# Performance work log

Measured on AMD Instinct MI355X. Metric: run time of the kernel, lower is better.

The kernel has to match this reference:

```python
import jax, jax.numpy as jnp
import numpy as np


def setup_inputs() -> dict:
    key = jax.random.key(0)
    k1, k2, k3 = jax.random.split(key, 3)
    B, C_IN, C_OUT, R, K = 4, 64, 64, 64, 3
    x = jax.random.normal(k1, (B, C_IN, R, R, R), dtype=jnp.float32)
    # per-voxel nonzero test |x|.sum(channel) != 0 used by the module)
    keep = jax.random.uniform(k2, (B, 1, R, R, R)) < 0.3
    x = x * keep.astype(jnp.float32)
    weight = jax.random.normal(k3, (C_OUT, C_IN, K, K, K), dtype=jnp.float32)
    return {"x": x, "weight": weight}


def reference(x, weight):
    # The torch module gathers a k^3 neighborhood at every nonzero input voxel,
    # contracts with the (unflipped) weight, and scatters to the same voxel.
    # This is exactly cross-correlation (torch conv semantics) with SAME padding,
    # masked to voxels where the input is nonzero across channels.
    K = weight.shape[-1]
    pad_l = K // 2
    pad_r = K - 1 - pad_l
    out = jax.lax.conv_general_dilated(
        x, weight,
        window_strides=(1, 1, 1),
        padding=[(pad_l, pad_r)] * 3,
        dimension_numbers=("NCDHW", "OIDHW", "NCDHW"),
    )  # [B, C_out, D, H, W]
    mask = (jnp.abs(x).sum(axis=1, keepdims=True) != 0)  # [B,1,D,H,W]
    return out * mask.astype(out.dtype)
```

## Files before the change

kernel.cpp:

```cpp
#include <hip/hip_runtime.h>
#include <stdint.h>


#define R3 262144
#define NVOX (4 * R3)
#define P  66
#define PS (66 * 66)
#define PB (66 * 66 * 66)
#define WSW_ELEMS (27 * 2 * 4 * 64 * 8)
#define CAP (NVOX / 2)

typedef __attribute__((ext_vector_type(4))) float f32x4;
typedef __attribute__((ext_vector_type(8))) short short8;

static __device__ inline unsigned short f2bf(float f) {
    union { float f; unsigned u; } v; v.f = f;
    unsigned u = v.u;
    return (unsigned short)((u + 0x7fffu + ((u >> 16) & 1u)) >> 16);
}

static __device__ __forceinline__ void gload16(const void* g, void* l) {
    __builtin_amdgcn_global_load_lds(
        (const __attribute__((address_space(1))) unsigned int*)g,
        (__attribute__((address_space(3))) unsigned int*)l, 16, 0, 0);
}

__global__ void wprep(const float* __restrict__ w, unsigned short* __restrict__ wsw) {
    int e = blockIdx.x * 256 + threadIdx.x;
    if (e >= WSW_ELEMS) return;
    int j    = e & 7;
    int lane = (e >> 3) & 63;
    int nt   = (e >> 9) & 3;
    int kc   = (e >> 11) & 1;
    int tap  = e >> 12;
    int co = nt * 16 + (lane & 15);
    int ci = kc * 32 + ((lane >> 4) * 8) + j;
    wsw[e] = f2bf(w[(co * 64 + ci) * 27 + tap]);
}

__global__ void __launch_bounds__(256) halo_zero(uint4* __restrict__ xt4) {
    int p = blockIdx.x * 256 + threadIdx.x;
    if (p >= 4 * PB) return;
    int b = p / PB;
    int rp = p - b * PB;
    int z = rp / PS; rp -= z * PS;
    int y = rp / P;  int xx = rp - y * P;
    if (z == 0 || z == 65 || y == 0 || y == 65 || xx == 0 || xx == 65) {
        uint4 zz = {0, 0, 0, 0};
        uint4* d = xt4 + (size_t)p * 8;
#pragma unroll
        for (int k = 0; k < 8; ++k) d[k] = zz;
    }
}

__global__ void __launch_bounds__(256) xprep(const float* __restrict__ x,
                                             unsigned int* __restrict__ xt_u32,
                                             int* __restrict__ list,
                                             int* __restrict__ pos,
                                             int* __restrict__ count) {
    __shared__ unsigned int lds[256 * 36];
    __shared__ unsigned int wcnt[4], wbase[4], bbase;
    int t = threadIdx.x;
    int v = blockIdx.x * 256 + t;
    int b = v >> 18;
    int s = v & (R3 - 1);
    const float* xb = x + (size_t)b * (64 * R3) + s;
    bool active = false;
    unsigned int pk[32];
#pragma unroll
    for (int c2 = 0; c2 < 32; ++c2) {
        float f0 = xb[(size_t)(2 * c2) * R3];
        float f1 = xb[(size_t)(2 * c2 + 1) * R3];
        active |= (f0 != 0.f) | (f1 != 0.f);
        pk[c2] = (unsigned)f2bf(f0) | ((unsigned)f2bf(f1) << 16);
    }
#pragma unroll
    for (int k = 0; k < 8; ++k) {
        uint4 q = { pk[4 * k], pk[4 * k + 1], pk[4 * k + 2], pk[4 * k + 3] };
        *(uint4*)&lds[t * 36 + 4 * k] = q;
    }
    __syncthreads();
    int s0 = (blockIdx.x * 256) & (R3 - 1);
    int z0 = s0 >> 12;
    int y0 = (s0 >> 6) & 63;
    size_t rowbase = ((size_t)b * PB + (size_t)(z0 + 1) * PS + (size_t)(y0 + 1) * P + 1) * 32;
#pragma unroll
    for (int i = 0; i < 8; ++i) {
        int g4 = i * 256 + t;
        int vox = g4 >> 3;
        int col = (g4 & 7) * 4;
        uint4 val = *(const uint4*)&lds[vox * 36 + col];
        int r = vox >> 6;
        int xc = vox & 63;
        *(uint4*)&xt_u32[rowbase + (size_t)r * (P * 32) + (size_t)xc * 32 + col] = val;
    }
    int lane = t & 63, w = t >> 6;
    unsigned long long bal = __ballot(active);
    if (lane == 0) wcnt[w] = (unsigned)__popcll(bal);
    __syncthreads();
    if (t == 0) {
        unsigned tot = 0;
        for (int i = 0; i < 4; ++i) { wbase[i] = tot; tot += wcnt[i]; }
        bbase = (unsigned)atomicAdd(count, (int)tot);
    }
    __syncthreads();
    int p = -1;
    if (active) {
        unsigned pp = bbase + wbase[w] + (unsigned)__popcll(bal & ((1ULL << lane) - 1ULL));
        list[pp] = v;
        p = (int)pp;
    }
    pos[v] = p;
}

#define AST(tp, sl) do { if ((tp) < 27) {                                           \
    const int dz_ = (tp) / 9 - 1, dy_ = ((tp) / 3) % 3 - 1, dx_ = (tp) % 3 - 1;     \
    const ptrdiff_t dlt_ = (ptrdiff_t)(dz_ * PS + dy_ * P + dx_) * 128;             \
    _Pragma("unroll")                                                               \
    for (int i_ = 0; i_ < 4; ++i_)                                                  \
        gload16(asrc[i_] + dlt_, aw + (sl) * 4096 + i_ * 1024 + lane * 16);         \
    asm volatile("" ::: "memory");                                                  \
} } while (0)

#define BLD(tp, st) do { if ((tp) < 27) {                                           \
    _Pragma("unroll")                                                               \
    for (int j_ = 0; j_ < 8; ++j_)                                                  \
        breg[st][j_] = *(const short8*)(wswb + (size_t)(tp) * 8192 + j_ * 1024      \
                                        + lane * 16);                               \
    asm volatile("" ::: "memory");                                                  \
} } while (0)

__global__ void __launch_bounds__(256, 3) sconv_gemm(const unsigned char* __restrict__ xt,
                                                     const unsigned char* __restrict__ wswb,
                                                     const int* __restrict__ list,
                                                     const int* __restrict__ count_p,
                                                     float* __restrict__ out,
                                                     float* __restrict__ compact,
                                                     int use_compact) {
    __shared__ __align__(16) unsigned char Ab[4][3][4096];
    int count = *count_p;
    int nt_act = (count + 127) >> 7;
    int bid = blockIdx.x;
    if (bid >= nt_act) return;
    int qd = nt_act >> 3, rd = nt_act & 7;
    int xcd = bid & 7, ixx = bid >> 3;
    int tile = (xcd < rd ? xcd * (qd + 1) : rd * (qd + 1) + (xcd - rd) * qd) + ixx;
    int base = tile * 128;
    int t = threadIdx.x;
    int lane = t & 63, w = t >> 6;

    const unsigned char* asrc[4];
    {
        int seg = lane & 7;
        int rl0 = lane >> 3;
        int off = (seg * 16) ^ ((rl0 & 7) << 4);
#pragma unroll
        for (int i = 0; i < 4; ++i) {
            int gi = base + w * 32 + rl0 + 8 * i;
            int vid = (gi < count) ? list[gi] : 0;
            if (vid < 0) vid = 0;
            int bb = vid >> 18, sp = vid & (R3 - 1);
            int vz = sp >> 12, vy = (sp >> 6) & 63, vx = sp & 63;
            size_t pvox = (size_t)bb * PB + (size_t)(vz + 1) * PS + (size_t)(vy + 1) * P + (vx + 1);
            asrc[i] = xt + pvox * 128 + off;
        }
    }
    unsigned char* aw = &Ab[w][0][0];

    int cl = lane & 15;
    int hi16 = (lane >> 4) * 16;
    int aoff[2][2];
#pragma unroll
    for (int m = 0; m < 2; ++m)
#pragma unroll
        for (int kc = 0; kc < 2; ++kc)
            aoff[m][kc] = (m * 16 + cl) * 128 + ((kc * 64 + hi16) ^ ((cl & 7) << 4));

    f32x4 acc[2][4] = {};
    short8 breg[2][8];

    BLD(0, 0);
    AST(0, 0);
    AST(1, 1);
#pragma unroll
    for (int tp = 0; tp < 27; ++tp) {
        const int sl = tp % 3;
        const int st = tp & 1;
        if (tp == 0)       asm volatile("s_waitcnt vmcnt(4)"  ::: "memory");
        else if (tp < 26)  asm volatile("s_waitcnt vmcnt(12)" ::: "memory");
        else               asm volatile("s_waitcnt vmcnt(8)"  ::: "memory");
        short8 a0k0 = *(const short8*)(aw + sl * 4096 + aoff[0][0]);
        short8 a1k0 = *(const short8*)(aw + sl * 4096 + aoff[1][0]);
        short8 a0k1 = *(const short8*)(aw + sl * 4096 + aoff[0][1]);
        short8 a1k1 = *(const short8*)(aw + sl * 4096 + aoff[1][1]);
        BLD(tp + 1, st ^ 1);
        AST(tp + 2, (tp + 2) % 3);
#pragma unroll
        for (int n = 0; n < 4; ++n) {
            acc[0][n] = __builtin_amdgcn_mfma_f32_16x16x32_bf16(a0k0, breg[st][n], acc[0][n], 0, 0, 0);
            acc[1][n] = __builtin_amdgcn_mfma_f32_16x16x32_bf16(a1k0, breg[st][n], acc[1][n], 0, 0, 0);
        }
#pragma unroll
        for (int n = 0; n < 4; ++n) {
            acc[0][n] = __builtin_amdgcn_mfma_f32_16x16x32_bf16(a0k1, breg[st][4 + n], acc[0][n], 0, 0, 0);
            acc[1][n] = __builtin_amdgcn_mfma_f32_16x16x32_bf16(a1k1, breg[st][4 + n], acc[1][n], 0, 0, 0);
        }
        asm volatile("s_waitcnt lgkmcnt(0)" ::: "memory");
    }

    int q = lane >> 4;
    if (use_compact) {
#pragma unroll
        for (int m = 0; m < 2; ++m) {
#pragma unroll
            for (int rg = 0; rg < 4; ++rg) {
                int row = w * 32 + m * 16 + q * 4 + rg;
                int gi = base + row;
                if (gi < count && gi < CAP) {
#pragma unroll
                    for (int n = 0; n < 4; ++n)
                        compact[(size_t)gi * 64 + n * 16 + cl] = acc[m][n][rg];
                }
            }
        }
    } else {
#pragma unroll
        for (int m = 0; m < 2; ++m) {
#pragma unroll
            for (int rg = 0; rg < 4; ++rg) {
                int row = w * 32 + m * 16 + q * 4 + rg;
                int gi = base + row;
                if (gi < count) {
                    int vv = list[gi];
                    int bb2 = vv >> 18;
                    int sp = vv & (R3 - 1);
                    float* op = out + (size_t)(bb2 * 64 + cl) * R3 + sp;
#pragma unroll
                    for (int n = 0; n < 4; ++n)
                        op[(size_t)(n * 16) * R3] = acc[m][n][rg];
                }
            }
        }
    }
}

__global__ void __launch_bounds__(256) finalize(const uint4* __restrict__ compact4,
                                                const int* __restrict__ pos,
                                                float* __restrict__ out) {
    int t = threadIdx.x;
    int vb = blockIdx.x * 256;
    int b = vb >> 18;
    int sp0 = vb & (R3 - 1);
    int q = pos[vb + t];
    bool act = (unsigned)q < (unsigned)CAP;
    const uint4* src = compact4 + (size_t)(act ? q : 0) * 16;
    uint4 r[16];
#pragma unroll
    for (int s = 0; s < 16; ++s) {
        uint4 v = {0, 0, 0, 0};
        if (act) v = src[s];
        r[s] = v;
    }
    const float* rf = (const float*)r;
    float* ob = out + (size_t)b * 64 * R3 + sp0 + t;
#pragma unroll
    for (int co = 0; co < 64; ++co)
        ob[(size_t)co * R3] = rf[co];
}

__global__ void __launch_bounds__(64) fallback_conv(const float* __restrict__ x,
                                                    const float* __restrict__ wt,
                                                    float* __restrict__ out) {
    __shared__ float rowb[66];
    int bid = blockIdx.x;
    int y = bid & 63, z = (bid >> 6) & 63, co = (bid >> 12) & 63, b = bid >> 18;
    int t = threadIdx.x;
    float acc = 0.f;
    bool active = false;
    for (int ci = 0; ci < 64; ++ci) {
        const float* xp = x + ((size_t)(b * 64 + ci)) * R3;
        const float* wp = wt + ((size_t)(co * 64 + ci)) * 27;
        for (int dz = -1; dz <= 1; ++dz) {
            int nz = z + dz;
            bool okz = (unsigned)nz < 64u;
            for (int dy = -1; dy <= 1; ++dy) {
                int ny = y + dy;
                bool ok = okz && ((unsigned)ny < 64u);
                float v = ok ? xp[nz * 4096 + ny * 64 + t] : 0.f;
                rowb[t + 1] = v;
                if (t == 0) { rowb[0] = 0.f; rowb[65] = 0.f; }
                __syncthreads();
                if (dz == 0 && dy == 0) active |= (rowb[t + 1] != 0.f);
                const float* wq = wp + (dz + 1) * 9 + (dy + 1) * 3;
                acc += rowb[t] * wq[0] + rowb[t + 1] * wq[1] + rowb[t + 2] * wq[2];
                __syncthreads();
            }
        }
    }
    out[((size_t)(b * 64 + co)) * R3 + z * 4096 + y * 64 + t] = active ? acc : 0.f;
}

extern "C" void kernel_launch(void* const* d_in, const int* in_sizes, int n_in,
                              void* d_out, int out_size, void* d_ws, size_t ws_size,
                              hipStream_t stream) {
    const float* x = (const float*)d_in[0];
    const float* w = (const float*)d_in[1];
    float* out = (float*)d_out;

    const size_t XT_BYTES = (size_t)4 * PB * 128;
    const size_t LIST_OFF = XT_BYTES;
    const size_t POS_OFF  = LIST_OFF + (size_t)NVOX * 4;
    const size_t WSW_OFF  = POS_OFF + (size_t)NVOX * 4;
    const size_t CNT_OFF  = WSW_OFF + (size_t)WSW_ELEMS * 2;
    const size_t CMP_OFF  = (CNT_OFF + 256 + 255) & ~(size_t)255;
    const size_t NEED_S   = CMP_OFF;
    const size_t NEED_C   = CMP_OFF + (size_t)CAP * 64 * 4;

    if (ws_size < NEED_S) {
        fallback_conv<<<NVOX, 64, 0, stream>>>(x, w, out);
        return;
    }

    unsigned int*   xt   = (unsigned int*)d_ws;
    int*            list = (int*)((char*)d_ws + LIST_OFF);
    int*            pos  = (int*)((char*)d_ws + POS_OFF);
    unsigned short* wsw  = (unsigned short*)((char*)d_ws + WSW_OFF);
    int*            cnt  = (int*)((char*)d_ws + CNT_OFF);
    float*          cmp  = (float*)((char*)d_ws + CMP_OFF);
    int use_compact = (ws_size >= NEED_C) ? 1 : 0;

    hipMemsetAsync(cnt, 0, sizeof(int), stream);
    if (!use_compact)
        hipMemsetAsync(d_out, 0, (size_t)out_size * sizeof(float), stream);
    wprep<<<WSW_ELEMS / 256, 256, 0, stream>>>(w, wsw);
    halo_zero<<<(4 * PB + 255) / 256, 256, 0, stream>>>((uint4*)d_ws);
    xprep<<<NVOX / 256, 256, 0, stream>>>(x, xt, list, pos, cnt);
    sconv_gemm<<<NVOX / 128, 256, 0, stream>>>((const unsigned char*)xt,
                                               (const unsigned char*)wsw, list, cnt,
                                               out, cmp, use_compact);
    if (use_compact)
        finalize<<<NVOX / 256, 256, 0, stream>>>((const uint4*)cmp, pos, out);
}
```

Baseline: 683.0 us.

## Load A operands directly from global into registers, dropping LDS staging

The gathered activation rows are now loaded straight from global memory into MFMA operand registers with a three-slot register ring, in place of async global-to-LDS copies followed by LDS reads. Both A and B use a prefetch distance of two taps, and the manual vmcnt/lgkmcnt waits are removed, leaving scheduling to the compiler. This removes LDS traffic, the swizzle and the per-tap barriers-by-waitcnt, at the cost of more VGPRs: launch bounds drop from 3 to 2 blocks per SIMD, and the per-lane gather loads may be less coalesced.

Measured after the change: 730.1 us. +6.9%, slower.

```diff
diff --git a/kernel.cpp b/kernel.cpp
--- a/kernel.cpp
+++ b/kernel.cpp
@@ -17,12 +17,6 @@
     union { float f; unsigned u; } v; v.f = f;
     unsigned u = v.u;
     return (unsigned short)((u + 0x7fffu + ((u >> 16) & 1u)) >> 16);
-}
-
-static __device__ __forceinline__ void gload16(const void* g, void* l) {
-    __builtin_amdgcn_global_load_lds(
-        (const __attribute__((address_space(1))) unsigned int*)g,
-        (__attribute__((address_space(3))) unsigned int*)l, 16, 0, 0);
 }
 
 __global__ void wprep(const float* __restrict__ w, unsigned short* __restrict__ wsw) {
@@ -113,31 +107,31 @@
     pos[v] = p;
 }
 
-#define AST(tp, sl) do { if ((tp) < 27) {                                           \
+#define ALOAD(tp, sl) do { if ((tp) < 27) {                                         \
     const int dz_ = (tp) / 9 - 1, dy_ = ((tp) / 3) % 3 - 1, dx_ = (tp) % 3 - 1;     \
-    const ptrdiff_t dlt_ = (ptrdiff_t)(dz_ * PS + dy_ * P + dx_) * 128;             \
+    const int dlt_ = (dz_ * PS + dy_ * P + dx_) * 128;                              \
     _Pragma("unroll")                                                               \
-    for (int i_ = 0; i_ < 4; ++i_)                                                  \
-        gload16(asrc[i_] + dlt_, aw + (sl) * 4096 + i_ * 1024 + lane * 16);         \
-    asm volatile("" ::: "memory");                                                  \
+    for (int m_ = 0; m_ < 2; ++m_)                                                  \
+    _Pragma("unroll")                                                               \
+    for (int kc_ = 0; kc_ < 2; ++kc_)                                               \
+        a[sl][m_][kc_] = *(const short8*)(xt +                                      \
+            (size_t)(voffA[m_] + (unsigned)(dlt_ + kc_ * 64)));                     \
 } } while (0)
 
-#define BLD(tp, st) do { if ((tp) < 27) {                                           \
+#define BLOAD(tp, sl) do { if ((tp) < 27) {                                         \
     _Pragma("unroll")                                                               \
     for (int j_ = 0; j_ < 8; ++j_)                                                  \
-        breg[st][j_] = *(const short8*)(wswb + (size_t)(tp) * 8192 + j_ * 1024      \
-                                        + lane * 16);                               \
-    asm volatile("" ::: "memory");                                                  \
+        b[sl][j_] = *(const short8*)(wswb + (size_t)((tp) * 8192 + j_ * 1024)       \
+                                     + voffB);                                      \
 } } while (0)
 
-__global__ void __launch_bounds__(256, 3) sconv_gemm(const unsigned char* __restrict__ xt,
+__global__ void __launch_bounds__(256, 2) sconv_gemm(const unsigned char* __restrict__ xt,
                                                      const unsigned char* __restrict__ wswb,
                                                      const int* __restrict__ list,
                                                      const int* __restrict__ count_p,
                                                      float* __restrict__ out,
                                                      float* __restrict__ compact,
                                                      int use_compact) {
-    __shared__ __align__(16) unsigned char Ab[4][3][4096];
     int count = *count_p;
     int nt_act = (count + 127) >> 7;
     int bid = blockIdx.x;
@@ -145,67 +139,45 @@
     int qd = nt_act >> 3, rd = nt_act & 7;
     int xcd = bid & 7, ixx = bid >> 3;
     int tile = (xcd < rd ? xcd * (qd + 1) : rd * (qd + 1) + (xcd - rd) * qd) + ixx;
-    int base = tile * 128;
     int t = threadIdx.x;
     int lane = t & 63, w = t >> 6;
-
-    const unsigned char* asrc[4];
-    {
-        int seg = lane & 7;
-        int rl0 = lane >> 3;
-        int off = (seg * 16) ^ ((rl0 & 7) << 4);
-#pragma unroll
-        for (int i = 0; i < 4; ++i) {
-            int gi = base + w * 32 + rl0 + 8 * i;
-            int vid = (gi < count) ? list[gi] : 0;
-            if (vid < 0) vid = 0;
-            int bb = vid >> 18, sp = vid & (R3 - 1);
-            int vz = sp >> 12, vy = (sp >> 6) & 63, vx = sp & 63;
-            size_t pvox = (size_t)bb * PB + (size_t)(vz + 1) * PS + (size_t)(vy + 1) * P + (vx + 1);
-            asrc[i] = xt + pvox * 128 + off;
-        }
-    }
-    unsigned char* aw = &Ab[w][0][0];
-
+    int base = tile * 128 + w * 32;
     int cl = lane & 15;
     int hi16 = (lane >> 4) * 16;
-    int aoff[2][2];
-#pragma unroll
-    for (int m = 0; m < 2; ++m)
-#pragma unroll
-        for (int kc = 0; kc < 2; ++kc)
-            aoff[m][kc] = (m * 16 + cl) * 128 + ((kc * 64 + hi16) ^ ((cl & 7) << 4));
+
+    unsigned voffA[2];
+#pragma unroll
+    for (int m = 0; m < 2; ++m) {
+        int gi = base + m * 16 + cl;
+        int vid = (gi < count) ? list[gi] : 0;
+        int bb = vid >> 18, sp = vid & (R3 - 1);
+        int vz = sp >> 12, vy = (sp >> 6) & 63, vx = sp & 63;
+        voffA[m] = (unsigned)((bb * PB + (vz + 1) * PS + (vy + 1) * P + (vx + 1)) * 128)
+                   + (unsigned)hi16;
+    }
+    unsigned voffB = (unsigned)(lane * 16);
 
     f32x4 acc[2][4] = {};
-    short8 breg[2][8];
-
-    BLD(0, 0);
-    AST(0, 0);
-    AST(1, 1);
+    short8 a[3][2][2];
+    short8 b[3][8];
+
+    BLOAD(0, 0); ALOAD(0, 0);
+    BLOAD(1, 1); ALOAD(1, 1);
 #pragma unroll
     for (int tp = 0; tp < 27; ++tp) {
         const int sl = tp % 3;
-        const int st = tp & 1;
-        if (tp == 0)       asm volatile("s_waitcnt vmcnt(4)"  ::: "memory");
-        else if (tp < 26)  asm volatile("s_waitcnt vmcnt(12)" ::: "memory");
-        else               asm volatile("s_waitcnt vmcnt(8)"  ::: "memory");
-        short8 a0k0 = *(const short8*)(aw + sl * 4096 + aoff[0][0]);
-        short8 a1k0 = *(const short8*)(aw + sl * 4096 + aoff[1][0]);
-        short8 a0k1 = *(const short8*)(aw + sl * 4096 + aoff[0][1]);
-        short8 a1k1 = *(const short8*)(aw + sl * 4096 + aoff[1][1]);
-        BLD(tp + 1, st ^ 1);
-        AST(tp + 2, (tp + 2) % 3);
+        BLOAD(tp + 2, (tp + 2) % 3);
+        ALOAD(tp + 2, (tp + 2) % 3);
 #pragma unroll
         for (int n = 0; n < 4; ++n) {
-            acc[0][n] = __builtin_amdgcn_mfma_f32_16x16x32_bf16(a0k0, breg[st][n], acc[0][n], 0, 0, 0);
-            acc[1][n] = __builtin_amdgcn_mfma_f32_16x16x32_bf16(a1k0, breg[st][n], acc[1][n], 0, 0, 0);
+            acc[0][n] = __builtin_amdgcn_mfma_f32_16x16x32_bf16(a[sl][0][0], b[sl][n], acc[0][n], 0, 0, 0);
+            acc[1][n] = __builtin_amdgcn_mfma_f32_16x16x32_bf16(a[sl][1][0], b[sl][n], acc[1][n], 0, 0, 0);
         }
 #pragma unroll
         for (int n = 0; n < 4; ++n) {
-            acc[0][n] = __builtin_amdgcn_mfma_f32_16x16x32_bf16(a0k1, breg[st][4 + n], acc[0][n], 0, 0, 0);
-            acc[1][n] = __builtin_amdgcn_mfma_f32_16x16x32_bf16(a1k1, breg[st][4 + n], acc[1][n], 0, 0, 0);
-        }
-        asm volatile("s_waitcnt lgkmcnt(0)" ::: "memory");
+            acc[0][n] = __builtin_amdgcn_mfma_f32_16x16x32_bf16(a[sl][0][1], b[sl][4 + n], acc[0][n], 0, 0, 0);
+            acc[1][n] = __builtin_amdgcn_mfma_f32_16x16x32_bf16(a[sl][1][1], b[sl][4 + n], acc[1][n], 0, 0, 0);
+        }
     }
 
     int q = lane >> 4;
@@ -214,7 +186,7 @@
         for (int m = 0; m < 2; ++m) {
 #pragma unroll
             for (int rg = 0; rg < 4; ++rg) {
-                int row = w * 32 + m * 16 + q * 4 + rg;
+                int row = m * 16 + q * 4 + rg;
                 int gi = base + row;
                 if (gi < count && gi < CAP) {
 #pragma unroll
@@ -228,7 +200,7 @@
         for (int m = 0; m < 2; ++m) {
 #pragma unroll
             for (int rg = 0; rg < 4; ++rg) {
-                int row = w * 32 + m * 16 + q * 4 + rg;
+                int row = m * 16 + q * 4 + rg;
                 int gi = base + row;
                 if (gi < count) {
                     int vv = list[gi];
```
